# Performance work log

Hardware: AMD Instinct MI355X
Metric: run time of the kernel (lower is better)

The kernel has to match this reference:

```python
import jax, jax.numpy as jnp
import numpy as np

N = 50000
IN_F = 512
HID = 64
HEADS = 4
CLASSES = 6
E = 800000
NEG_SLOPE = 0.2


def setup_inputs() -> dict:
    key = jax.random.key(0)
    ks = jax.random.split(key, 12)
    s = 1.0 / np.sqrt(IN_F)
    s2 = 1.0 / np.sqrt(HID * HEADS)
    return {
        "x": jax.random.normal(ks[0], (N, IN_F), dtype=jnp.float32),
        "edge_index": jax.random.randint(ks[1], (2, E), 0, N, dtype=jnp.int32),
        "W1": jax.random.normal(ks[2], (IN_F, HEADS * HID), dtype=jnp.float32) * s,
        "a_src1": jax.random.normal(ks[3], (HEADS, HID), dtype=jnp.float32) * s,
        "a_dst1": jax.random.normal(ks[4], (HEADS, HID), dtype=jnp.float32) * s,
        "b1": jnp.zeros((HEADS * HID,), dtype=jnp.float32),
        "W2": jax.random.normal(ks[5], (HEADS * HID, CLASSES), dtype=jnp.float32) * s2,
        "a_src2": jax.random.normal(ks[6], (1, CLASSES), dtype=jnp.float32) * s2,
        "a_dst2": jax.random.normal(ks[7], (1, CLASSES), dtype=jnp.float32) * s2,
        "b2": jnp.zeros((CLASSES,), dtype=jnp.float32),
    }


def gat_conv(x, src, dst, W, a_src, a_dst, bias, heads, ch):
    # x: [N, F] -> h: [N, H, C]
    n = x.shape[0]
    h = (x @ W).reshape(n, heads, ch)
    # per-node attention halves: [N, H]
    e_src = jnp.einsum('nhc,hc->nh', h, a_src)
    e_dst = jnp.einsum('nhc,hc->nh', h, a_dst)
    # per-edge logits with leaky relu: [E', H]
    logits = jax.nn.leaky_relu(e_src[src] + e_dst[dst], NEG_SLOPE)
    # segment softmax over incoming edges of each dst node
    m = jax.ops.segment_max(logits, dst, num_segments=n)  # [N, H]
    p = jnp.exp(logits - m[dst])
    denom = jax.ops.segment_sum(p, dst, num_segments=n)   # [N, H] (>0: self loops)
    alpha = p / denom[dst]                                 # [E', H]
    # weighted scatter-aggregate: [N, H, C]
    out = jax.ops.segment_sum(alpha[:, :, None] * h[src], dst, num_segments=n)
    return out.reshape(n, heads * ch) + bias


def reference(x, edge_index, W1, a_src1, a_dst1, b1, W2, a_src2, a_dst2, b2):
    n = x.shape[0]
    loops = jnp.arange(n, dtype=edge_index.dtype)
    src = jnp.concatenate([edge_index[0], loops])  # PyG add_self_loops
    dst = jnp.concatenate([edge_index[1], loops])
    h = gat_conv(x, src, dst, W1, a_src1, a_dst1, b1, HEADS, HID)
    h = jax.nn.elu(h)
    out = gat_conv(h, src, dst, W2, a_src2, a_dst2, b2, 1, CLASSES)
    return jax.nn.log_softmax(out, axis=1)
```

## Files before the change

### kernel.cpp

```cpp
#include <hip/hip_runtime.h>

#define HEADS 4
#define HID 64
#define CH1 256
#define CLS 6
#define H2S 8
#define NSLOPE 0.2f

typedef short bf16x8 __attribute__((ext_vector_type(8)));
typedef float f32x4 __attribute__((ext_vector_type(4)));

__device__ __forceinline__ float leaky(float x) {
  return (x >= 0.f) ? x : NSLOPE * x;
}

__device__ __forceinline__ ushort f2bf(float f) {
  unsigned u = __float_as_uint(f);
  unsigned r = (u + 0x7FFFu + ((u >> 16) & 1u)) >> 16;
  return (ushort)r;
}

__device__ __forceinline__ float bf2f(ushort u) {
  return __uint_as_float((unsigned)u << 16);
}

__device__ __forceinline__ void gload16(const void* g, void* l) {
  __builtin_amdgcn_global_load_lds((const __attribute__((address_space(1))) void*)g,
                                   (__attribute__((address_space(3))) void*)l, 16, 0, 0);
}

__global__ void k_cvt_w1t(const float* __restrict__ W1, ushort* __restrict__ w1t) {
  int t = blockIdx.x * 256 + threadIdx.x;
  if (t >= 512 * 256) return;
  int k = t >> 8, c = t & 255;
  w1t[c * 512 + k] = f2bf(W1[t]);
}

__global__ __launch_bounds__(256) void k_gemm1_mfma(
    const float* __restrict__ x,
    const ushort* __restrict__ w1t,
    const float* __restrict__ a_src, const float* __restrict__ a_dst,
    ushort* __restrict__ h1b, float* __restrict__ es, float* __restrict__ ed,
    int M) {
  __shared__ ushort ldsA[2][2048];
  __shared__ ushort ldsB[2][8192];
  int t = threadIdx.x;
  int wid = t >> 6, lane = t & 63;
  int brow = blockIdx.x * 64;

  int rA = t >> 2, qA = t & 3, lsA = qA ^ (rA & 3);
  int rowA = brow + rA; if (rowA >= M) rowA = M - 1;
  const float* srcA = x + (size_t)rowA * 512 + lsA * 8;
  int dAw = t * 8;

  int cB = t >> 2;
  int sB = (t & 3) ^ (cB & 3);
  const ushort* srcB0 = w1t + (size_t)cB * 512 + sB * 8;
  int dB = t * 8;

  int l15 = lane & 15, g = lane >> 4;
  int sw = ((g ^ (lane & 3)) << 3);
  int aoff[4], boff[4];
#pragma unroll
  for (int m = 0; m < 4; ++m) aoff[m] = (m * 16 + l15) * 32 + sw;
#pragma unroll
  for (int n = 0; n < 4; ++n) boff[n] = (wid * 64 + n * 16 + l15) * 32 + sw;

  f32x4 acc[4][4] = {};
  f32x4 aLo, aHi;

#define LOADA(kt) do { \
    aLo = *(const f32x4*)(srcA + (kt) * 32); \
    aHi = *(const f32x4*)(srcA + (kt) * 32 + 4); \
  } while (0)

#define WRITEA(buf) do { \
    union { unsigned u[4]; bf16x8 b; } cv; \
    asm("v_cvt_pk_bf16_f32 %0, %1, %2" : "=v"(cv.u[0]) : "v"(aLo[0]), "v"(aLo[1])); \
    asm("v_cvt_pk_bf16_f32 %0, %1, %2" : "=v"(cv.u[1]) : "v"(aLo[2]), "v"(aLo[3])); \
    asm("v_cvt_pk_bf16_f32 %0, %1, %2" : "=v"(cv.u[2]) : "v"(aHi[0]), "v"(aHi[1])); \
    asm("v_cvt_pk_bf16_f32 %0, %1, %2" : "=v"(cv.u[3]) : "v"(aHi[2]), "v"(aHi[3])); \
    *(bf16x8*)&ldsA[buf][dAw] = cv.b; \
  } while (0)

#define STAGEB(buf, kt) do { \
    gload16(srcB0 + (kt) * 32,             &ldsB[buf][dB]); \
    gload16(srcB0 +  64 * 512 + (kt) * 32, &ldsB[buf][dB + 2048]); \
    gload16(srcB0 + 128 * 512 + (kt) * 32, &ldsB[buf][dB + 4096]); \
    gload16(srcB0 + 192 * 512 + (kt) * 32, &ldsB[buf][dB + 6144]); \
  } while (0)

  LOADA(0);
  STAGEB(0, 0);
  WRITEA(0);
  __syncthreads();

  int cur = 0;
  for (int kt = 0; kt < 16; ++kt) {
    if (kt < 15) {
      LOADA(kt + 1);
      STAGEB(cur ^ 1, kt + 1);
    }
    bf16x8 av[4], bv[4];
#pragma unroll
    for (int m = 0; m < 4; ++m) av[m] = *(const bf16x8*)&ldsA[cur][aoff[m]];
#pragma unroll
    for (int n = 0; n < 4; ++n) bv[n] = *(const bf16x8*)&ldsB[cur][boff[n]];
#pragma unroll
    for (int m = 0; m < 4; ++m)
#pragma unroll
      for (int n = 0; n < 4; ++n)
        acc[m][n] = __builtin_amdgcn_mfma_f32_16x16x32_bf16(av[m], bv[n], acc[m][n], 0, 0, 0);
    if (kt < 15) WRITEA(cur ^ 1);
    __syncthreads();
    cur ^= 1;
  }
#undef LOADA
#undef WRITEA
#undef STAGEB

  float as4[4], ad4[4];
#pragma unroll
  for (int n = 0; n < 4; ++n) {
    int c = wid * 64 + n * 16 + l15;
    as4[n] = a_src[c];
    ad4[n] = a_dst[c];
  }
  int rbase = g * 4;
#pragma unroll
  for (int m = 0; m < 4; ++m) {
#pragma unroll
    for (int r = 0; r < 4; ++r) {
      int grow = brow + m * 16 + rbase + r;
      bool ok = grow < M;
      float ps = 0.f, pd = 0.f;
#pragma unroll
      for (int n = 0; n < 4; ++n) {
        float v = acc[m][n][r];
        ps += v * as4[n];
        pd += v * ad4[n];
        if (ok) h1b[(size_t)grow * CH1 + wid * 64 + n * 16 + l15] = f2bf(v);
      }
#pragma unroll
      for (int o = 1; o < 16; o <<= 1) {
        ps += __shfl_xor(ps, o);
        pd += __shfl_xor(pd, o);
      }
      if (l15 == 0 && ok) {
        es[grow * HEADS + wid] = ps;
        ed[grow * HEADS + wid] = pd;
      }
    }
  }
}

__global__ void k_count(const int* __restrict__ ei, int E, int Etot,
                        int* __restrict__ cnt) {
  int e = blockIdx.x * blockDim.x + threadIdx.x;
  if (e >= Etot) return;
  int d = (e < E) ? ei[E + e] : e - E;
  atomicAdd(&cnt[d], 1);
}

__global__ __launch_bounds__(256) void k_scan1(const int* __restrict__ deg,
    int* __restrict__ rowptr, int* __restrict__ bsum, int n) {
  int i = blockIdx.x * 256 + threadIdx.x;
  int v = (i < n) ? deg[i] : 0;
  int lane = threadIdx.x & 63, wave = threadIdx.x >> 6;
  int incl = v;
#pragma unroll
  for (int o = 1; o < 64; o <<= 1) {
    int u = __shfl_up(incl, o);
    if (lane >= o) incl += u;
  }
  __shared__ int ws4[4];
  if (lane == 63) ws4[wave] = incl;
  __syncthreads();
  if (threadIdx.x == 0) {
    int run = 0;
    for (int w = 0; w < 4; ++w) { int x = ws4[w]; ws4[w] = run; run += x; }
    bsum[blockIdx.x] = run;
  }
  __syncthreads();
  if (i < n) rowptr[i] = incl - v + ws4[wave];
}

__global__ __launch_bounds__(256) void k_scan2(int* __restrict__ bsum, int nb) {
  int t = threadIdx.x;
  int v = (t < nb) ? bsum[t] : 0;
  int lane = t & 63, wave = t >> 6;
  int incl = v;
#pragma unroll
  for (int o = 1; o < 64; o <<= 1) {
    int u = __shfl_up(incl, o);
    if (lane >= o) incl += u;
  }
  __shared__ int ws4[4];
  if (lane == 63) ws4[wave] = incl;
  __syncthreads();
  if (t == 0) {
    int run = 0;
    for (int w = 0; w < 4; ++w) { int x = ws4[w]; ws4[w] = run; run += x; }
  }
  __syncthreads();
  if (t < nb) bsum[t] = incl - v + ws4[wave];
}

__global__ void k_scan3(int* __restrict__ rowptr, const int* __restrict__ bsum,
                        int n, int Etot) {
  int i = blockIdx.x * 256 + threadIdx.x;
  if (i < n) rowptr[i] += bsum[blockIdx.x];
  if (i == 0) rowptr[n] = Etot;
}

__global__ void k_scatter(const int* __restrict__ ei, int E, int Etot,
    const int* __restrict__ rowptr, int* __restrict__ cursor,
    int* __restrict__ esrc) {
  int e = blockIdx.x * blockDim.x + threadIdx.x;
  if (e >= Etot) return;
  int s, d;
  if (e < E) { s = ei[e]; d = ei[E + e]; } else { s = d = e - E; }
  int pos = rowptr[d] + atomicAdd(&cursor[d], 1);
  esrc[pos] = s;
}

__global__ __launch_bounds__(256) void k_agg1_csr(const int* __restrict__ rowptr,
    const int* __restrict__ esrc, const float* __restrict__ es,
    const float* __restrict__ ed, const ushort* __restrict__ h1b,
    const float* __restrict__ b1, float* __restrict__ out1, int Nn) {
  __shared__ int   spi[4][64];
  __shared__ float spp[4][64 * 4];
  int wid = threadIdx.x >> 6, lane = threadIdx.x & 63;
  int d = blockIdx.x * 4 + wid;
  if (d >= Nn) return;
  int beg = rowptr[d], end = rowptr[d + 1];
  float4 edv = *(const float4*)&ed[d * 4];
  int myhead = lane >> 4;
  int ch = lane * 4;
  const char* hcb = (const char*)h1b + (size_t)ch * 2;

  float4 m4 = make_float4(-1e30f, -1e30f, -1e30f, -1e30f);
  for (int i = beg + lane; i < end; i += 64) {
    int s = esrc[i];
    float4 e4 = *(const float4*)&es[s * 4];
    m4.x = fmaxf(m4.x, leaky(e4.x + edv.x));
    m4.y = fmaxf(m4.y, leaky(e4.y + edv.y));
    m4.z = fmaxf(m4.z, leaky(e4.z + edv.z));
    m4.w = fmaxf(m4.w, leaky(e4.w + edv.w));
  }
#pragma unroll
  for (int o = 32; o; o >>= 1) {
    m4.x = fmaxf(m4.x, __shfl_xor(m4.x, o));
    m4.y = fmaxf(m4.y, __shfl_xor(m4.y, o));
    m4.z = fmaxf(m4.z, __shfl_xor(m4.z, o));
    m4.w = fmaxf(m4.w, __shfl_xor(m4.w, o));
  }

  float4 acc = make_float4(0.f, 0.f, 0.f, 0.f);
  float4 den4 = make_float4(0.f, 0.f, 0.f, 0.f);
  const float* pp = &spp[wid][0];
  for (int c0 = beg; c0 < end; c0 += 64) {
    int i = c0 + lane;
    int s = 0;
    float4 p = make_float4(0.f, 0.f, 0.f, 0.f);
    if (i < end) {
      s = esrc[i];
      float4 e4 = *(const float4*)&es[s * 4];
      p.x = __expf(leaky(e4.x + edv.x) - m4.x);
      p.y = __expf(leaky(e4.y + edv.y) - m4.y);
      p.z = __expf(leaky(e4.z + edv.z) - m4.z);
      p.w = __expf(leaky(e4.w + edv.w) - m4.w);
    }
    den4.x += p.x; den4.y += p.y; den4.z += p.z; den4.w += p.w;
    spi[wid][lane] = s << 9;
    *(float4*)&spp[wid][lane * 4] = p;
    int cl = min(64, end - c0);
    int j = 0;
    for (; j + 3 < cl; j += 4) {
      int o0 = spi[wid][j],     o1 = spi[wid][j + 1];
      int o2 = spi[wid][j + 2], o3 = spi[wid][j + 3];
      float p0 = pp[j * 4 + myhead],       p1 = pp[(j + 1) * 4 + myhead];
      float p2 = pp[(j + 2) * 4 + myhead], p3 = pp[(j + 3) * 4 + myhead];
      ushort4 v0 = *(const ushort4*)(hcb + o0);
      ushort4 v1 = *(const ushort4*)(hcb + o1);
      ushort4 v2 = *(const ushort4*)(hcb + o2);
      ushort4 v3 = *(const ushort4*)(hcb + o3);
      acc.x += p0 * bf2f(v0.x) + p1 * bf2f(v1.x) + p2 * bf2f(v2.x) + p3 * bf2f(v3.x);
      acc.y += p0 * bf2f(v0.y) + p1 * bf2f(v1.y) + p2 * bf2f(v2.y) + p3 * bf2f(v3.y);
      acc.z += p0 * bf2f(v0.z) + p1 * bf2f(v1.z) + p2 * bf2f(v2.z) + p3 * bf2f(v3.z);
      acc.w += p0 * bf2f(v0.w) + p1 * bf2f(v1.w) + p2 * bf2f(v2.w) + p3 * bf2f(v3.w);
    }
    for (; j < cl; ++j) {
      int oj = spi[wid][j];
      float pj = pp[j * 4 + myhead];
      ushort4 v = *(const ushort4*)(hcb + oj);
      acc.x += pj * bf2f(v.x);
      acc.y += pj * bf2f(v.y);
      acc.z += pj * bf2f(v.z);
      acc.w += pj * bf2f(v.w);
    }
  }
#pragma unroll
  for (int o = 32; o; o >>= 1) {
    den4.x += __shfl_xor(den4.x, o);
    den4.y += __shfl_xor(den4.y, o);
    den4.z += __shfl_xor(den4.z, o);
    den4.w += __shfl_xor(den4.w, o);
  }
  float den = (myhead == 0) ? den4.x : (myhead == 1) ? den4.y
            : (myhead == 2) ? den4.z : den4.w;
  float4 b4 = *(const float4*)&b1[ch];
  float4 r;
  r.x = acc.x / den + b4.x; r.x = (r.x > 0.f) ? r.x : expm1f(r.x);
  r.y = acc.y / den + b4.y; r.y = (r.y > 0.f) ? r.y : expm1f(r.y);
  r.z = acc.z / den + b4.z; r.z = (r.z > 0.f) ? r.z : expm1f(r.z);
  r.w = acc.w / den + b4.w; r.w = (r.w > 0.f) ? r.w : expm1f(r.w);
  *(float4*)&out1[(size_t)d * CH1 + ch] = r;
}

__global__ __launch_bounds__(256) void k_gemm2(const float* __restrict__ h,
    const float* __restrict__ W2, const float* __restrict__ a_src2,
    const float* __restrict__ a_dst2, float* __restrict__ h2,
    float* __restrict__ es2, float* __restrict__ ed2, int Nn) {
  __shared__ float w[CH1][CLS];
  for (int i = threadIdx.x; i < CH1 * CLS; i += 256)
    w[i / CLS][i % CLS] = W2[i];
  __syncthreads();
  int n = blockIdx.x * 256 + threadIdx.x;
  if (n >= Nn) return;
  const float* hr = &h[(size_t)n * CH1];
  float a0 = 0.f, a1 = 0.f, a2 = 0.f, a3 = 0.f, a4 = 0.f, a5 = 0.f;
#pragma unroll 8
  for (int k = 0; k < CH1; k += 4) {
    float4 x = *(const float4*)&hr[k];
    a0 += x.x * w[k][0] + x.y * w[k + 1][0] + x.z * w[k + 2][0] + x.w * w[k + 3][0];
    a1 += x.x * w[k][1] + x.y * w[k + 1][1] + x.z * w[k + 2][1] + x.w * w[k + 3][1];
    a2 += x.x * w[k][2] + x.y * w[k + 1][2] + x.z * w[k + 2][2] + x.w * w[k + 3][2];
    a3 += x.x * w[k][3] + x.y * w[k + 1][3] + x.z * w[k + 2][3] + x.w * w[k + 3][3];
    a4 += x.x * w[k][4] + x.y * w[k + 1][4] + x.z * w[k + 2][4] + x.w * w[k + 3][4];
    a5 += x.x * w[k][5] + x.y * w[k + 1][5] + x.z * w[k + 2][5] + x.w * w[k + 3][5];
  }
  float* h2r = &h2[(size_t)n * H2S];
  h2r[0] = a0; h2r[1] = a1; h2r[2] = a2; h2r[3] = a3; h2r[4] = a4; h2r[5] = a5;
  es2[n] = a0 * a_src2[0] + a1 * a_src2[1] + a2 * a_src2[2]
         + a3 * a_src2[3] + a4 * a_src2[4] + a5 * a_src2[5];
  ed2[n] = a0 * a_dst2[0] + a1 * a_dst2[1] + a2 * a_dst2[2]
         + a3 * a_dst2[3] + a4 * a_dst2[4] + a5 * a_dst2[5];
}

__global__ __launch_bounds__(256) void k_l2(const int* __restrict__ rowptr,
    const int* __restrict__ esrc, const float* __restrict__ es2,
    const float* __restrict__ ed2, const float* __restrict__ h2,
    const float* __restrict__ b2, float* __restrict__ out, int Nn) {
  int t = threadIdx.x;
  int grp = t >> 3, sl = t & 7;
  int n = blockIdx.x * 32 + grp;
  if (n >= Nn) return;
  int beg = rowptr[n], end = rowptr[n + 1];
  float edv = ed2[n];
  float m = -1e30f;
  for (int i = beg + sl; i < end; i += 8)
    m = fmaxf(m, leaky(es2[esrc[i]] + edv));
  m = fmaxf(m, __shfl_xor(m, 1));
  m = fmaxf(m, __shfl_xor(m, 2));
  m = fmaxf(m, __shfl_xor(m, 4));
  float den = 0.f, a0 = 0.f, a1 = 0.f, a2 = 0.f, a3 = 0.f, a4 = 0.f, a5 = 0.f;
  for (int i = beg + sl; i < end; i += 8) {
    int s = esrc[i];
    float p = __expf(leaky(es2[s] + edv) - m);
    den += p;
    const float* hr = &h2[(size_t)s * H2S];
    float4 v0 = *(const float4*)hr;
    float2 v1 = *(const float2*)(hr + 4);
    a0 += p * v0.x; a1 += p * v0.y; a2 += p * v0.z;
    a3 += p * v0.w; a4 += p * v1.x; a5 += p * v1.y;
  }
#pragma unroll
  for (int o = 1; o < 8; o <<= 1) {
    den += __shfl_xor(den, o);
    a0 += __shfl_xor(a0, o); a1 += __shfl_xor(a1, o); a2 += __shfl_xor(a2, o);
    a3 += __shfl_xor(a3, o); a4 += __shfl_xor(a4, o); a5 += __shfl_xor(a5, o);
  }
  if (sl == 0) {
    float v[CLS];
    v[0] = a0 / den + b2[0]; v[1] = a1 / den + b2[1]; v[2] = a2 / den + b2[2];
    v[3] = a3 / den + b2[3]; v[4] = a4 / den + b2[4]; v[5] = a5 / den + b2[5];
    float mx = -1e30f;
#pragma unroll
    for (int j = 0; j < CLS; ++j) mx = fmaxf(mx, v[j]);
    float sum = 0.f;
#pragma unroll
    for (int j = 0; j < CLS; ++j) sum += __expf(v[j] - mx);
    float l = mx + logf(sum);
#pragma unroll
    for (int j = 0; j < CLS; ++j) out[n * CLS + j] = v[j] - l;
  }
}

extern "C" void kernel_launch(void* const* d_in, const int* in_sizes, int n_in,
                              void* d_out, int out_size, void* d_ws, size_t ws_size,
                              hipStream_t stream) {
  const float* x      = (const float*)d_in[0];
  const int*   ei     = (const int*)d_in[1];
  const float* W1     = (const float*)d_in[2];
  const float* a_src1 = (const float*)d_in[3];
  const float* a_dst1 = (const float*)d_in[4];
  const float* b1     = (const float*)d_in[5];
  const float* W2     = (const float*)d_in[6];
  const float* a_src2 = (const float*)d_in[7];
  const float* a_dst2 = (const float*)d_in[8];
  const float* b2     = (const float*)d_in[9];
  float* out = (float*)d_out;

  const int IN_F = 512;
  int N = in_sizes[0] / IN_F;
  int E = in_sizes[1] / 2;
  int Etot = E + N;

  float* ws = (float*)d_ws;
  size_t off = 0;
  ushort* h1b = (ushort*)(ws + off); off += (size_t)N * CH1;
  float* out1 = ws + off; off += (size_t)N * CH1;
  float* es1  = ws + off; off += (size_t)N * HEADS;
  float* ed1  = ws + off; off += (size_t)N * HEADS;
  float* h2   = ws + off; off += (size_t)N * H2S;
  float* es2  = ws + off; off += (size_t)N;
  float* ed2  = ws + off; off += (size_t)N;
  int* rowptr = (int*)(ws + off); off += (size_t)N + 1;
  int* cursor = (int*)(ws + off); off += (size_t)N;
  int* bsum   = (int*)(ws + off); off += 256;
  int* esrc   = (int*)(ws + off); off += (size_t)Etot;
  ushort* w1t = (ushort*)(ws + off); off += (512 * 256 * 2 + 3) / 4;

  int nb = (N + 255) / 256;
  int eb = (Etot + 255) / 256;

  hipMemsetAsync(cursor, 0, (size_t)N * 4, stream);
  k_count<<<eb, 256, 0, stream>>>(ei, E, Etot, cursor);
  k_scan1<<<nb, 256, 0, stream>>>(cursor, rowptr, bsum, N);
  k_scan2<<<1, 256, 0, stream>>>(bsum, nb);
  k_scan3<<<nb, 256, 0, stream>>>(rowptr, bsum, N, Etot);
  hipMemsetAsync(cursor, 0, (size_t)N * 4, stream);
  k_scatter<<<eb, 256, 0, stream>>>(ei, E, Etot, rowptr, cursor, esrc);

  k_cvt_w1t<<<(512 * 256 + 255) / 256, 256, 0, stream>>>(W1, w1t);
  k_gemm1_mfma<<<(N + 63) / 64, 256, 0, stream>>>(x, w1t, a_src1, a_dst1,
                                                  h1b, es1, ed1, N);
  k_agg1_csr<<<(N + 3) / 4, 256, 0, stream>>>(rowptr, esrc, es1, ed1, h1b, b1, out1, N);

  k_gemm2<<<(N + 255) / 256, 256, 0, stream>>>(out1, W2, a_src2, a_dst2,
                                               h2, es2, ed2, N);
  k_l2<<<(N + 31) / 32, 256, 0, stream>>>(rowptr, esrc, es2, ed2, h2, b2, out, N);
}
```

Baseline: 266.2 us.

## Fuse layer-2 projection into aggregation, load W1 from registers, drop memset

The layer-2 linear projection and attention-score computation move into the layer-1 aggregation kernel. Each wave multiplies its ELU output by W2 held in registers and reduces across the wave, so the 50000x256 fp32 intermediate is no longer written and re-read and one launch disappears. The GEMM1 B operand is now loaded straight from global memory into registers with a double buffer instead of being staged through LDS. The degree counter is zeroed inside the scan kernel, which removes the second memset. The trade-offs are more VGPR pressure in both kernels and uncoalesced B loads that rely on cache.

```diff
diff --git a/kernel.cpp b/kernel.cpp
--- a/kernel.cpp
+++ b/kernel.cpp
@@ -22,11 +22,6 @@
 
 __device__ __forceinline__ float bf2f(ushort u) {
   return __uint_as_float((unsigned)u << 16);
-}
-
-__device__ __forceinline__ void gload16(const void* g, void* l) {
-  __builtin_amdgcn_global_load_lds((const __attribute__((address_space(1))) void*)g,
-                                   (__attribute__((address_space(3))) void*)l, 16, 0, 0);
 }
 
 __global__ void k_cvt_w1t(const float* __restrict__ W1, ushort* __restrict__ w1t) {
@@ -43,7 +38,6 @@
     ushort* __restrict__ h1b, float* __restrict__ es, float* __restrict__ ed,
     int M) {
   __shared__ ushort ldsA[2][2048];
-  __shared__ ushort ldsB[2][8192];
   int t = threadIdx.x;
   int wid = t >> 6, lane = t & 63;
   int brow = blockIdx.x * 64;
@@ -53,18 +47,16 @@
   const float* srcA = x + (size_t)rowA * 512 + lsA * 8;
   int dAw = t * 8;
 
-  int cB = t >> 2;
-  int sB = (t & 3) ^ (cB & 3);
-  const ushort* srcB0 = w1t + (size_t)cB * 512 + sB * 8;
-  int dB = t * 8;
-
   int l15 = lane & 15, g = lane >> 4;
   int sw = ((g ^ (lane & 3)) << 3);
-  int aoff[4], boff[4];
+  int aoff[4];
 #pragma unroll
   for (int m = 0; m < 4; ++m) aoff[m] = (m * 16 + l15) * 32 + sw;
-#pragma unroll
-  for (int n = 0; n < 4; ++n) boff[n] = (wid * 64 + n * 16 + l15) * 32 + sw;
+
+  const ushort* bp[4];
+#pragma unroll
+  for (int n = 0; n < 4; ++n)
+    bp[n] = w1t + (size_t)(wid * 64 + n * 16 + l15) * 512 + g * 8;
 
   f32x4 acc[4][4] = {};
   f32x4 aLo, aHi;
@@ -83,41 +75,35 @@
     *(bf16x8*)&ldsA[buf][dAw] = cv.b; \
   } while (0)
 
-#define STAGEB(buf, kt) do { \
-    gload16(srcB0 + (kt) * 32,             &ldsB[buf][dB]); \
-    gload16(srcB0 +  64 * 512 + (kt) * 32, &ldsB[buf][dB + 2048]); \
-    gload16(srcB0 + 128 * 512 + (kt) * 32, &ldsB[buf][dB + 4096]); \
-    gload16(srcB0 + 192 * 512 + (kt) * 32, &ldsB[buf][dB + 6144]); \
-  } while (0)
-
+  bf16x8 bv[2][4];
+#pragma unroll
+  for (int n = 0; n < 4; ++n) bv[0][n] = *(const bf16x8*)bp[n];
   LOADA(0);
-  STAGEB(0, 0);
   WRITEA(0);
   __syncthreads();
 
-  int cur = 0;
+#pragma unroll
   for (int kt = 0; kt < 16; ++kt) {
+    const int cur = kt & 1;
     if (kt < 15) {
       LOADA(kt + 1);
-      STAGEB(cur ^ 1, kt + 1);
+#pragma unroll
+      for (int n = 0; n < 4; ++n)
+        bv[(kt + 1) & 1][n] = *(const bf16x8*)(bp[n] + (kt + 1) * 32);
     }
-    bf16x8 av[4], bv[4];
+    bf16x8 av[4];
 #pragma unroll
     for (int m = 0; m < 4; ++m) av[m] = *(const bf16x8*)&ldsA[cur][aoff[m]];
 #pragma unroll
-    for (int n = 0; n < 4; ++n) bv[n] = *(const bf16x8*)&ldsB[cur][boff[n]];
-#pragma unroll
     for (int m = 0; m < 4; ++m)
 #pragma unroll
       for (int n = 0; n < 4; ++n)
-        acc[m][n] = __builtin_amdgcn_mfma_f32_16x16x32_bf16(av[m], bv[n], acc[m][n], 0, 0, 0);
+        acc[m][n] = __builtin_amdgcn_mfma_f32_16x16x32_bf16(av[m], bv[cur][n], acc[m][n], 0, 0, 0);
     if (kt < 15) WRITEA(cur ^ 1);
     __syncthreads();
-    cur ^= 1;
   }
 #undef LOADA
 #undef WRITEA
-#undef STAGEB
 
   float as4[4], ad4[4];
 #pragma unroll
@@ -162,10 +148,11 @@
   atomicAdd(&cnt[d], 1);
 }
 
-__global__ __launch_bounds__(256) void k_scan1(const int* __restrict__ deg,
+__global__ __launch_bounds__(256) void k_scan1(int* __restrict__ deg,
     int* __restrict__ rowptr, int* __restrict__ bsum, int n) {
   int i = blockIdx.x * 256 + threadIdx.x;
   int v = (i < n) ? deg[i] : 0;
+  if (i < n) deg[i] = 0;
   int lane = threadIdx.x & 63, wave = threadIdx.x >> 6;
   int incl = v;
 #pragma unroll
@@ -227,16 +214,26 @@
 __global__ __launch_bounds__(256) void k_agg1_csr(const int* __restrict__ rowptr,
     const int* __restrict__ esrc, const float* __restrict__ es,
     const float* __restrict__ ed, const ushort* __restrict__ h1b,
-    const float* __restrict__ b1, float* __restrict__ out1, int Nn) {
+    const float* __restrict__ b1, const float* __restrict__ W2,
+    const float* __restrict__ a_src2, const float* __restrict__ a_dst2,
+    float* __restrict__ h2, float* __restrict__ es2, float* __restrict__ ed2,
+    int Nn) {
   __shared__ int   spi[4][64];
   __shared__ float spp[4][64 * 4];
   int wid = threadIdx.x >> 6, lane = threadIdx.x & 63;
+  int ch = lane * 4;
+  float w2s[4][CLS];
+#pragma unroll
+  for (int c = 0; c < 4; ++c)
+#pragma unroll
+    for (int j = 0; j < CLS; ++j)
+      w2s[c][j] = W2[(ch + c) * CLS + j];
+
   int d = blockIdx.x * 4 + wid;
   if (d >= Nn) return;
   int beg = rowptr[d], end = rowptr[d + 1];
   float4 edv = *(const float4*)&ed[d * 4];
   int myhead = lane >> 4;
-  int ch = lane * 4;
   const char* hcb = (const char*)h1b + (size_t)ch * 2;
 
   float4 m4 = make_float4(-1e30f, -1e30f, -1e30f, -1e30f);
@@ -315,37 +312,26 @@
   r.y = acc.y / den + b4.y; r.y = (r.y > 0.f) ? r.y : expm1f(r.y);
   r.z = acc.z / den + b4.z; r.z = (r.z > 0.f) ? r.z : expm1f(r.z);
   r.w = acc.w / den + b4.w; r.w = (r.w > 0.f) ? r.w : expm1f(r.w);
-  *(float4*)&out1[(size_t)d * CH1 + ch] = r;
-}
-
-__global__ __launch_bounds__(256) void k_gemm2(const float* __restrict__ h,
-    const float* __restrict__ W2, const float* __restrict__ a_src2,
-    const float* __restrict__ a_dst2, float* __restrict__ h2,
-    float* __restrict__ es2, float* __restrict__ ed2, int Nn) {
-  __shared__ float w[CH1][CLS];
-  for (int i = threadIdx.x; i < CH1 * CLS; i += 256)
-    w[i / CLS][i % CLS] = W2[i];
-  __syncthreads();
-  int n = blockIdx.x * 256 + threadIdx.x;
-  if (n >= Nn) return;
-  const float* hr = &h[(size_t)n * CH1];
-  float a0 = 0.f, a1 = 0.f, a2 = 0.f, a3 = 0.f, a4 = 0.f, a5 = 0.f;
-#pragma unroll 8
-  for (int k = 0; k < CH1; k += 4) {
-    float4 x = *(const float4*)&hr[k];
-    a0 += x.x * w[k][0] + x.y * w[k + 1][0] + x.z * w[k + 2][0] + x.w * w[k + 3][0];
-    a1 += x.x * w[k][1] + x.y * w[k + 1][1] + x.z * w[k + 2][1] + x.w * w[k + 3][1];
-    a2 += x.x * w[k][2] + x.y * w[k + 1][2] + x.z * w[k + 2][2] + x.w * w[k + 3][2];
-    a3 += x.x * w[k][3] + x.y * w[k + 1][3] + x.z * w[k + 2][3] + x.w * w[k + 3][3];
-    a4 += x.x * w[k][4] + x.y * w[k + 1][4] + x.z * w[k + 2][4] + x.w * w[k + 3][4];
-    a5 += x.x * w[k][5] + x.y * w[k + 1][5] + x.z * w[k + 2][5] + x.w * w[k + 3][5];
-  }
-  float* h2r = &h2[(size_t)n * H2S];
-  h2r[0] = a0; h2r[1] = a1; h2r[2] = a2; h2r[3] = a3; h2r[4] = a4; h2r[5] = a5;
-  es2[n] = a0 * a_src2[0] + a1 * a_src2[1] + a2 * a_src2[2]
-         + a3 * a_src2[3] + a4 * a_src2[4] + a5 * a_src2[5];
-  ed2[n] = a0 * a_dst2[0] + a1 * a_dst2[1] + a2 * a_dst2[2]
-         + a3 * a_dst2[3] + a4 * a_dst2[4] + a5 * a_dst2[5];
+
+  float q0 = r.x * w2s[0][0] + r.y * w2s[1][0] + r.z * w2s[2][0] + r.w * w2s[3][0];
+  float q1 = r.x * w2s[0][1] + r.y * w2s[1][1] + r.z * w2s[2][1] + r.w * w2s[3][1];
+  float q2 = r.x * w2s[0][2] + r.y * w2s[1][2] + r.z * w2s[2][2] + r.w * w2s[3][2];
+  float q3 = r.x * w2s[0][3] + r.y * w2s[1][3] + r.z * w2s[2][3] + r.w * w2s[3][3];
+  float q4 = r.x * w2s[0][4] + r.y * w2s[1][4] + r.z * w2s[2][4] + r.w * w2s[3][4];
+  float q5 = r.x * w2s[0][5] + r.y * w2s[1][5] + r.z * w2s[2][5] + r.w * w2s[3][5];
+#pragma unroll
+  for (int o = 32; o; o >>= 1) {
+    q0 += __shfl_xor(q0, o); q1 += __shfl_xor(q1, o); q2 += __shfl_xor(q2, o);
+    q3 += __shfl_xor(q3, o); q4 += __shfl_xor(q4, o); q5 += __shfl_xor(q5, o);
+  }
+  if (lane == 0) {
+    float* h2r = &h2[(size_t)d * H2S];
+    h2r[0] = q0; h2r[1] = q1; h2r[2] = q2; h2r[3] = q3; h2r[4] = q4; h2r[5] = q5;
+    es2[d] = q0 * a_src2[0] + q1 * a_src2[1] + q2 * a_src2[2]
+           + q3 * a_src2[3] + q4 * a_src2[4] + q5 * a_src2[5];
+    ed2[d] = q0 * a_dst2[0] + q1 * a_dst2[1] + q2 * a_dst2[2]
+           + q3 * a_dst2[3] + q4 * a_dst2[4] + q5 * a_dst2[5];
+  }
 }
 
 __global__ __launch_bounds__(256) void k_l2(const int* __restrict__ rowptr,
@@ -420,7 +406,6 @@
   float* ws = (float*)d_ws;
   size_t off = 0;
   ushort* h1b = (ushort*)(ws + off); off += (size_t)N * CH1;
-  float* out1 = ws + off; off += (size_t)N * CH1;
   float* es1  = ws + off; off += (size_t)N * HEADS;
   float* ed1  = ws + off; off += (size_t)N * HEADS;
   float* h2   = ws + off; off += (size_t)N * H2S;
@@ -440,15 +425,13 @@
   k_scan1<<<nb, 256, 0, stream>>>(cursor, rowptr, bsum, N);
   k_scan2<<<1, 256, 0, stream>>>(bsum, nb);
   k_scan3<<<nb, 256, 0, stream>>>(rowptr, bsum, N, Etot);
-  hipMemsetAsync(cursor, 0, (size_t)N * 4, stream);
   k_scatter<<<eb, 256, 0, stream>>>(ei, E, Etot, rowptr, cursor, esrc);
 
   k_cvt_w1t<<<(512 * 256 + 255) / 256, 256, 0, stream>>>(W1, w1t);
   k_gemm1_mfma<<<(N + 63) / 64, 256, 0, stream>>>(x, w1t, a_src1, a_dst1,
                                                   h1b, es1, ed1, N);
-  k_agg1_csr<<<(N + 3) / 4, 256, 0, stream>>>(rowptr, esrc, es1, ed1, h1b, b1, out1, N);
-
-  k_gemm2<<<(N + 255) / 256, 256, 0, stream>>>(out1, W2, a_src2, a_dst2,
-                                               h2, es2, ed2, N);
+  k_agg1_csr<<<(N + 3) / 4, 256, 0, stream>>>(rowptr, esrc, es1, ed1, h1b, b1,
+                                              W2, a_src2, a_dst2, h2, es2, ed2, N);
+
   k_l2<<<(N + 31) / 32, 256, 0, stream>>>(rowptr, esrc, es2, ed2, h2, b2, out, N);
 }
```

New measurement: 260.8 us. 1.02x faster.
